# Optimization experiments

Measured on AMD Instinct MI355X. Metric: run time of the kernel, lower is better.

## Reference

```python
import jax, jax.numpy as jnp
import numpy as np
import math

B, T = 512, 512
ENC = 512          # 2 * input_size
N_MELS, R = 80, 2
ATTN, DEC = 256, 256
PRE_H, PRE_O = 256, 256
HID = 128          # DCA hidden
SC, SK = 8, 21     # static channels / kernel
DC, DK = 8, 21     # dynamic channels / kernel
PL, PA, PB = 11, 0.1, 0.9  # prior length, alpha, beta


def _betabinom_pmf(k, n, a, b):
    lg = math.lgamma
    return math.exp(lg(n + 1) - lg(k + 1) - lg(n - k + 1)
                    + lg(k + a) + lg(n - k + b) - lg(n + a + b)
                    - (lg(a) + lg(b) - lg(a + b)))


def setup_inputs() -> dict:
    key = jax.random.key(0)
    ks = iter(jax.random.split(key, 64))
    def rn(shape, s=0.05):
        return jax.random.normal(next(ks), shape, dtype=jnp.float32) * s
    inp = {}
    inp["h"] = rn([B, T, ENC], 1.0)
    inp["y"] = rn([B, N_MELS], 1.0)
    a = jax.random.uniform(next(ks), [B, T], dtype=jnp.float32)
    inp["alpha"] = a / a.sum(-1, keepdims=True)  # valid attention distribution
    inp["c"] = rn([B, ENC], 1.0)
    for n in ["attn_h0", "attn_c0", "rnn1_h0", "rnn1_c0", "rnn2_h0", "rnn2_c0"]:
        inp[n] = rn([B, ATTN], 1.0)
    # prenet
    inp["fc1_w"] = rn([PRE_H, N_MELS]); inp["fc1_b"] = rn([PRE_H])
    inp["fc2_w"] = rn([PRE_O, PRE_H]); inp["fc2_b"] = rn([PRE_O])
    # dynamic convolution attention
    inp["W_w"] = rn([HID, ATTN]); inp["W_b"] = rn([HID])
    inp["V_w"] = rn([DC * DK, HID])
    inp["F_w"] = rn([SC, 1, SK])
    inp["U_w"] = rn([HID, SC])
    inp["T_w"] = rn([HID, DC]); inp["T_b"] = rn([HID])
    inp["v_w"] = rn([1, HID])
    P = np.array([_betabinom_pmf(k, PL - 1, PA, PB) for k in range(PL)], np.float32)[::-1].copy()
    inp["P"] = jnp.asarray(P)
    # attn LSTM cell: input = 2*input_size + prenet output = 768
    inp["attn_wih"] = rn([4 * ATTN, ENC + PRE_O]); inp["attn_whh"] = rn([4 * ATTN, ATTN])
    inp["attn_bih"] = rn([4 * ATTN]); inp["attn_bhh"] = rn([4 * ATTN])
    inp["lin_w"] = rn([DEC, ENC + ATTN]); inp["lin_b"] = rn([DEC])
    for pfx in ["r1", "r2"]:
        inp[pfx + "_wih"] = rn([4 * DEC, DEC]); inp[pfx + "_whh"] = rn([4 * DEC, DEC])
        inp[pfx + "_bih"] = rn([4 * DEC]); inp[pfx + "_bhh"] = rn([4 * DEC])
    inp["proj_w"] = rn([N_MELS * R, DEC])
    return inp


def _lstm(x, h, c, wih, whh, bih, bhh):
    g = x @ wih.T + bih + h @ whh.T + bhh
    i, f, gg, o = jnp.split(g, 4, axis=-1)
    c2 = jax.nn.sigmoid(f) * c + jax.nn.sigmoid(i) * jnp.tanh(gg)
    return jax.nn.sigmoid(o) * jnp.tanh(c2), c2


def _win(x, k):
    # x: [B, T + k - 1] padded signal -> sliding windows [B, T, k]
    idx = jnp.arange(T)[:, None] + jnp.arange(k)[None, :]
    return x[:, idx]


def reference(h, y, alpha, c, attn_h0, attn_c0, rnn1_h0, rnn1_c0, rnn2_h0, rnn2_c0,
              fc1_w, fc1_b, fc2_w, fc2_b, W_w, W_b, V_w, F_w, U_w, T_w, T_b, v_w, P,
              attn_wih, attn_whh, attn_bih, attn_bhh, lin_w, lin_b,
              r1_wih, r1_whh, r1_bih, r1_bhh, r2_wih, r2_whh, r2_bih, r2_bhh, proj_w):
    # prenet (eval mode -> dropout inactive since fixed=False)
    yp = jax.nn.relu(jax.nn.relu(y @ fc1_w.T + fc1_b) @ fc2_w.T + fc2_b)
    attn_h, attn_c = _lstm(jnp.concatenate([c, yp], -1), attn_h0, attn_c0,
                           attn_wih, attn_whh, attn_bih, attn_bhh)
    # --- dynamic convolution attention ---
    # prior: causal conv with flipped beta-binomial pmf
    p = jnp.einsum('btk,k->bt', _win(jnp.pad(alpha, ((0, 0), (PL - 1, 0))), PL), P)
    p = jnp.log(jnp.clip(p, 1e-6))
    # dynamic filters per batch element: [B, DC, DK]
    G = (jnp.tanh(attn_h @ W_w.T + W_b) @ V_w.T).reshape(-1, DC, DK)
    wd = _win(jnp.pad(alpha, ((0, 0), ((DK - 1) // 2, (DK - 1) // 2))), DK)  # [B,T,DK]
    g = jnp.einsum('btk,bck->btc', wd, G)  # grouped conv1d, groups=B
    ws = _win(jnp.pad(alpha, ((0, 0), ((SK - 1) // 2, (SK - 1) // 2))), SK)
    f = jnp.einsum('btk,ck->btc', ws, F_w[:, 0, :])  # static conv1d
    e = jnp.squeeze(jnp.tanh(f @ U_w.T + g @ T_w.T + T_b) @ v_w.T, -1) + p
    alpha2 = jax.nn.softmax(e, axis=-1)
    # --- context + decoder stack ---
    c2 = jnp.einsum('bt,btd->bd', alpha2, h)
    x = jnp.concatenate([c2, attn_h], -1) @ lin_w.T + lin_b
    r1_h, r1_c = _lstm(x, rnn1_h0, rnn1_c0, r1_wih, r1_whh, r1_bih, r1_bhh)
    x = x + r1_h
    r2_h, r2_c = _lstm(x, rnn2_h0, rnn2_c0, r2_wih, r2_whh, r2_bih, r2_bhh)
    x = x + r2_h
    out = (x @ proj_w.T).reshape(-1, N_MELS, R)
    return (out, alpha2, c2, attn_h, attn_c, r1_h, r1_c, r2_h, r2_c)
```

## Files before the change

kernel.cpp:

```cpp
#include <hip/hip_runtime.h>

typedef unsigned short u16;
typedef __attribute__((ext_vector_type(8))) short s8v;
typedef __attribute__((ext_vector_type(4))) float f32x4;

__device__ __forceinline__ float bf2f(u16 u) { return __uint_as_float(((unsigned)u) << 16); }
__device__ __forceinline__ u16 f2bf(float f) {
    unsigned u = __float_as_uint(f);
    return (u16)((u + 0x7fffu + ((u >> 16) & 1u)) >> 16);
}
__device__ __forceinline__ float ldraw(const void* p, size_t i, int dt) {
    return dt ? ((const float*)p)[i] : bf2f(((const u16*)p)[i]);
}
__device__ __forceinline__ int fl(const int* F, int f) { return f < 0 ? 1 : F[f]; }
__device__ __forceinline__ float fast_tanh(float x) {
    x = fminf(fmaxf(x, -15.f), 15.f);
    float e = __expf(2.f * x);
    return (e - 1.f) / (e + 1.f);
}
__device__ __forceinline__ float sigm(float x) { return 1.f / (1.f + __expf(-x)); }

__global__ __launch_bounds__(256) void k_detect(int* __restrict__ flagsRaw,
    const void* p0, const void* p1, const void* p2, const void* p3, const void* p4,
    const void* p5, const void* p6, const void* p7, const void* p8, const void* p9,
    const void* p10, const void* p11, const void* p12, const void* p13, const void* p14,
    const void* p15, const void* p16, const void* p17, const void* p18, const void* p19,
    const void* p20, const void* p21, const void* p22, const void* p23, const void* p24,
    const void* p25, const void* p26, const void* p27, const void* p28, const void* p29,
    const void* p30, const void* p31, const void* p32, const void* p33, const void* p34,
    const void* p35, const void* p36, const void* p37)
{
    const void* ptrs[38] = {p0,p1,p2,p3,p4,p5,p6,p7,p8,p9,p10,p11,p12,p13,p14,p15,p16,
                            p17,p18,p19,p20,p21,p22,p23,p24,p25,p26,p27,p28,p29,p30,p31,
                            p32,p33,p34,p35,p36,p37};
    const int ns[38] = {134217728, 40960, 262144, 262144,
                        131072,131072,131072,131072,131072,131072,
                        20480,256,65536,256,
                        32768,128,21504,168,1024,1024,128,128,11,
                        786432,262144,1024,1024, 196608,256,
                        262144,262144,1024,1024, 262144,262144,1024,1024, 40960};
    __shared__ int s;
    int b = blockIdx.x, tid = threadIdx.x;
    if (tid == 0) s = 0;
    __syncthreads();
    int nsamp = ns[b] >> 1;
    if (nsamp > 512) nsamp = 512;
    const u16* q = (const u16*)ptrs[b];
    int bad = 0;
    for (int i = tid; i < nsamp; i += 256) {
        u16 u = q[2 * i];
        int e = (u >> 7) & 0xff;
        bad += (e < 96 || e > 159) ? 1 : 0;
    }
    atomicAdd(&s, bad);
    __syncthreads();
    if (tid == 0) flagsRaw[b] = (s * 4 > nsamp) ? 1 : 0;
}

__global__ __launch_bounds__(256) void k_finish(
    const int* __restrict__ FRAW, int* __restrict__ FF,
    const void* U_w, const void* T_w, const void* T_b, const void* v_w, const void* F_w,
    float* utw, float* tbf, float* vf, float* ff)
{
    __shared__ int sflag[38];
    const int big[38] = {1,1,1,1, 1,1,1,1,1,1, 1,0,1,0,
                         1,0,1,0,1,1,0,0,0, 1,1,1,1, 1,0,
                         1,1,1,1, 1,1,1,1, 1};
    int tid = threadIdx.x;
    if (tid == 0) {
        int s = 0, c = 0;
        for (int i = 0; i < 38; i++) if (big[i]) { s += FRAW[i]; c++; }
        int maj = (s * 2 > c) ? 1 : 0;
        for (int i = 0; i < 38; i++) { int v = big[i] ? FRAW[i] : maj; sflag[i] = v; FF[i] = v; }
    }
    __syncthreads();
    int dU = sflag[18], dT = sflag[19], dTb = sflag[20], dV = sflag[21], dF = sflag[17];
    for (int i = tid; i < 1024; i += 256) {
        int j = i >> 3, c = i & 7;
        utw[j * 16 + c]     = ldraw(U_w, i, dU);
        utw[j * 16 + 8 + c] = ldraw(T_w, i, dT);
    }
    if (tid < 128) { tbf[tid] = ldraw(T_b, tid, dTb); vf[tid] = ldraw(v_w, tid, dV); }
    if (tid < 168) ff[tid] = ldraw(F_w, tid, dF);
}

__device__ __forceinline__ void vg32_pair(const int* F,
    const void* A, int lda, int fa, const void* B, int ldb, int bo, int fb, int K,
    int m0, int n0, int N, int tid, int tx, int ty, float* acc,
    float (*As)[68], float (*Bs)[68])
{
    int dA = fl(F, fa), dB = fl(F, fb);
    bool fastp = dA && dB;
    for (int k0 = 0; k0 < K; k0 += 64) {
        __syncthreads();
        if (fastp) {
            #pragma unroll
            for (int p = 0; p < 2; p++) {
                int e = tid + p * 256;
                int row = e >> 4, kk = (e & 15) * 4;
                float4 va = {0.f, 0.f, 0.f, 0.f};
                if (k0 + kk < K)
                    va = *(const float4*)((const float*)A + (size_t)(m0 + row) * lda + k0 + kk);
                *(float4*)&As[row][kk] = va;
                int nr = n0 + row;
                float4 vb = {0.f, 0.f, 0.f, 0.f};
                if (nr < N && k0 + kk < K)
                    vb = *(const float4*)((const float*)B + (size_t)nr * ldb + bo + k0 + kk);
                *(float4*)&Bs[row][kk] = vb;
            }
        } else {
            #pragma unroll
            for (int p = 0; p < 8; p++) {
                int e = tid + p * 256;
                int row = e >> 6, kk = e & 63;
                As[row][kk] = (k0 + kk < K) ? ldraw(A, (size_t)(m0 + row) * lda + k0 + kk, dA) : 0.f;
                int nr = n0 + row;
                Bs[row][kk] = (nr < N && k0 + kk < K)
                            ? ldraw(B, (size_t)nr * ldb + bo + k0 + kk, dB) : 0.f;
            }
        }
        __syncthreads();
        #pragma unroll
        for (int kq = 0; kq < 16; kq++) {
            float4 a0 = *(const float4*)&As[ty][kq * 4];
            float4 a1 = *(const float4*)&As[ty + 16][kq * 4];
            float4 b0 = *(const float4*)&Bs[tx][kq * 4];
            float4 b1 = *(const float4*)&Bs[tx + 16][kq * 4];
            acc[0] += a0.x*b0.x + a0.y*b0.y + a0.z*b0.z + a0.w*b0.w;
            acc[1] += a0.x*b1.x + a0.y*b1.y + a0.z*b1.z + a0.w*b1.w;
            acc[2] += a1.x*b0.x + a1.y*b0.y + a1.z*b0.z + a1.w*b0.w;
            acc[3] += a1.x*b1.x + a1.y*b1.y + a1.z*b1.z + a1.w*b1.w;
        }
    }
}

__global__ __launch_bounds__(256) void k_vgemm32(
    const int* __restrict__ F,
    const void* A1, int lda1, int fa1, const void* B1, int ldb1, int bo1, int fb1, int K1,
    const void* A2, int lda2, int fa2, const void* B2, int ldb2, int bo2, int fb2, int K2,
    const void* bias1, int fx1,
    float* __restrict__ Cf, int ldc, int N, int act)
{
    __shared__ float As[32][68], Bs[32][68];
    int tid = threadIdx.x, tx = tid & 15, ty = tid >> 4;
    int m0 = blockIdx.y * 32, n0 = blockIdx.x * 32;
    float acc[4] = {0.f, 0.f, 0.f, 0.f};
    vg32_pair(F, A1, lda1, fa1, B1, ldb1, bo1, fb1, K1, m0, n0, N, tid, tx, ty, acc, As, Bs);
    if (A2) vg32_pair(F, A2, lda2, fa2, B2, ldb2, bo2, fb2, K2, m0, n0, N, tid, tx, ty, acc, As, Bs);

    #pragma unroll
    for (int c = 0; c < 2; c++) {
        int n = n0 + tx + c * 16;
        if (n >= N) continue;
        float bias = 0.f;
        if (bias1) bias += ldraw(bias1, n, fl(F, fx1));
        #pragma unroll
        for (int r = 0; r < 2; r++) {
            float v = acc[r * 2 + c] + bias;
            if (act == 1) v = fmaxf(v, 0.f);
            else if (act == 2) v = fast_tanh(v);
            Cf[(size_t)(m0 + ty + r * 16) * ldc + n] = v;
        }
    }
}

__global__ __launch_bounds__(256) void k_lin(
    const int* __restrict__ F, const float* __restrict__ part, float* __restrict__ o_c2,
    const float* __restrict__ ah, const void* lin_w, const void* lin_b,
    float* __restrict__ x1f)
{
    __shared__ float As[32][68], Bs[32][68];
    int tid = threadIdx.x, tx = tid & 15, ty = tid >> 4;
    int m0 = blockIdx.y * 32, n0 = blockIdx.x * 32;
    int dB = fl(F, 27);
    float acc[4] = {0.f, 0.f, 0.f, 0.f};
    for (int k0 = 0; k0 < 512; k0 += 64) {
        __syncthreads();
        #pragma unroll
        for (int p = 0; p < 2; p++) {
            int e = tid + p * 256;
            int row = e >> 4, kk = (e & 15) * 4;
            size_t idx = (size_t)(m0 + row) * 512 + k0 + kk;
            float4 va = *(const float4*)(part + idx);
            float4 vb2 = *(const float4*)(part + idx + 262144);
            va.x += vb2.x; va.y += vb2.y; va.z += vb2.z; va.w += vb2.w;
            *(float4*)&As[row][kk] = va;
            if (blockIdx.x == 0) *(float4*)(o_c2 + idx) = va;
            int nr = n0 + row;
            float4 vb;
            if (dB) {
                vb = *(const float4*)((const float*)lin_w + (size_t)nr * 768 + k0 + kk);
            } else {
                const u16* q = (const u16*)lin_w + (size_t)nr * 768 + k0 + kk;
                vb.x = bf2f(q[0]); vb.y = bf2f(q[1]); vb.z = bf2f(q[2]); vb.w = bf2f(q[3]);
            }
            *(float4*)&Bs[row][kk] = vb;
        }
        __syncthreads();
        #pragma unroll
        for (int kq = 0; kq < 16; kq++) {
            float4 a0 = *(const float4*)&As[ty][kq * 4];
            float4 a1 = *(const float4*)&As[ty + 16][kq * 4];
            float4 b0 = *(const float4*)&Bs[tx][kq * 4];
            float4 b1 = *(const float4*)&Bs[tx + 16][kq * 4];
            acc[0] += a0.x*b0.x + a0.y*b0.y + a0.z*b0.z + a0.w*b0.w;
            acc[1] += a0.x*b1.x + a0.y*b1.y + a0.z*b1.z + a0.w*b1.w;
            acc[2] += a1.x*b0.x + a1.y*b0.y + a1.z*b0.z + a1.w*b0.w;
            acc[3] += a1.x*b1.x + a1.y*b1.y + a1.z*b1.z + a1.w*b1.w;
        }
    }
    vg32_pair(F, ah, 256, -1, lin_w, 768, 512, 27, 256, m0, n0, 256, tid, tx, ty, acc, As, Bs);

    int dbias = fl(F, 28);
    #pragma unroll
    for (int c = 0; c < 2; c++) {
        int n = n0 + tx + c * 16;
        float bias = ldraw(lin_b, n, dbias);
        #pragma unroll
        for (int r = 0; r < 2; r++)
            x1f[(size_t)(m0 + ty + r * 16) * 256 + n] = acc[r * 2 + c] + bias;
    }
}

__device__ __forceinline__ void lstm_mfma_piece(const int* F,
    const void* A, int lda, int fa, const void* B, int ldb, int bo, int fb, int K,
    int b0, int j0, int tid, int wave, int lane, f32x4& acc,
    u16 (*As)[72], u16 (*Bs)[72])
{
    int dA = fl(F, fa), dB = fl(F, fb);
    for (int k0 = 0; k0 < K; k0 += 64) {
        __syncthreads();
        for (int g = tid; g < 640; g += 256) {
            const void* src; int dt; size_t idx; u16* dst;
            if (g < 128) {
                int row = g >> 3, kg = (g & 7) * 8;
                idx = (size_t)(b0 + row) * lda + k0 + kg;
                src = A; dt = dA; dst = &As[row][kg];
            } else {
                int gb = g - 128;
                int row = gb >> 3, kg = (gb & 7) * 8;
                int grow = (row >> 4) * 256 + j0 + (row & 15);
                idx = (size_t)grow * ldb + bo + k0 + kg;
                src = B; dt = dB; dst = &Bs[row][kg];
            }
            if (dt) {
                const float* sp = (const float*)src + idx;
                float4 a = *(const float4*)sp;
                float4 b = *(const float4*)(sp + 4);
                s8v v;
                v[0] = (short)f2bf(a.x); v[1] = (short)f2bf(a.y);
                v[2] = (short)f2bf(a.z); v[3] = (short)f2bf(a.w);
                v[4] = (short)f2bf(b.x); v[5] = (short)f2bf(b.y);
                v[6] = (short)f2bf(b.z); v[7] = (short)f2bf(b.w);
                *(s8v*)dst = v;
            } else {
                *(s8v*)dst = *(const s8v*)((const u16*)src + idx);
            }
        }
        __syncthreads();
        int r = lane & 15, kg = (lane >> 4) * 8;
        s8v a0 = *(const s8v*)&As[r][kg];
        s8v w0 = *(const s8v*)&Bs[wave * 16 + r][kg];
        acc = __builtin_amdgcn_mfma_f32_16x16x32_bf16(a0, w0, acc, 0, 0, 0);
        s8v a1 = *(const s8v*)&As[r][32 + kg];
        s8v w1 = *(const s8v*)&Bs[wave * 16 + r][32 + kg];
        acc = __builtin_amdgcn_mfma_f32_16x16x32_bf16(a1, w1, acc, 0, 0, 0);
    }
}

__global__ __launch_bounds__(256) void k_lstm(
    const int* __restrict__ F,
    const void* A1, int lda1, int fa1, const void* B1, int ldb1, int bo1, int fb1, int K1,
    const void* A2, int lda2, int fa2, const void* B2, int ldb2, int bo2, int fb2, int K2,
    const void* A3, int lda3, int fa3, const void* B3, int ldb3, int bo3, int fb3, int K3,
    const void* bih, int fx1, const void* bhh, int fx2,
    const void* c0, int fc0,
    float* __restrict__ h_out, float* __restrict__ c_out,
    const float* __restrict__ xprev, float* __restrict__ xout)
{
    __shared__ u16 As[16][72];
    __shared__ u16 Bs[64][72];
    __shared__ float sG[4][16][16];
    int tid = threadIdx.x, lane = tid & 63, wave = tid >> 6;
    int j0 = blockIdx.x * 16, b0 = blockIdx.y * 16;
    f32x4 acc = {0.f, 0.f, 0.f, 0.f};
    lstm_mfma_piece(F, A1, lda1, fa1, B1, ldb1, bo1, fb1, K1, b0, j0, tid, wave, lane, acc, As, Bs);
    if (A2) lstm_mfma_piece(F, A2, lda2, fa2, B2, ldb2, bo2, fb2, K2, b0, j0, tid, wave, lane, acc, As, Bs);
    if (A3) lstm_mfma_piece(F, A3, lda3, fa3, B3, ldb3, bo3, fb3, K3, b0, j0, tid, wave, lane, acc, As, Bs);

    #pragma unroll
    for (int r2 = 0; r2 < 4; r2++)
        sG[wave][(lane >> 4) * 4 + r2][lane & 15] = acc[r2];
    __syncthreads();

    int jl = tid & 15, bl = tid >> 4;
    int j = j0 + jl, b = b0 + bl;
    int dx1 = fl(F, fx1), dx2 = fl(F, fx2);
    float gi = sG[0][bl][jl] + ldraw(bih, j, dx1)       + ldraw(bhh, j, dx2);
    float gf = sG[1][bl][jl] + ldraw(bih, j + 256, dx1) + ldraw(bhh, j + 256, dx2);
    float gg = sG[2][bl][jl] + ldraw(bih, j + 512, dx1) + ldraw(bhh, j + 512, dx2);
    float go = sG[3][bl][jl] + ldraw(bih, j + 768, dx1) + ldraw(bhh, j + 768, dx2);
    size_t idx = (size_t)b * 256 + j;
    float cp = ldraw(c0, idx, F[fc0]);
    float cn = sigm(gf) * cp + sigm(gi) * fast_tanh(gg);
    float hn = sigm(go) * fast_tanh(cn);
    h_out[idx] = hn;
    c_out[idx] = cn;
    if (xprev) xout[idx] = xprev[idx] + hn;
}

__global__ __launch_bounds__(256) void k_dca(
    const int* __restrict__ F, const void* __restrict__ alpha, const void* __restrict__ P,
    const float* __restrict__ G, const float* __restrict__ utw, const float* __restrict__ tbf,
    const float* __restrict__ vf, const float* __restrict__ ff,
    float* __restrict__ o_a2)
{
    __shared__ float4 sut[512];
    __shared__ float stb[128], sv[128], sff[168], sgd[168], sal[532], spf[16], sred[8];
    int dA = F[2], dP = F[22];
    int b = blockIdx.x, tid = threadIdx.x;
    for (int i = tid; i < 512; i += 256) sut[i] = ((const float4*)utw)[i];
    if (tid < 128) { stb[tid] = tbf[tid]; sv[tid] = vf[tid]; }
    if (tid < 168) { sff[tid] = ff[tid]; sgd[tid] = G[(size_t)b * 168 + tid]; }
    if (tid < 11)  spf[tid] = ldraw(P, tid, dP);
    for (int i = tid; i < 532; i += 256)
        sal[i] = (i >= 10 && i < 522) ? ldraw(alpha, (size_t)b * 512 + i - 10, dA) : 0.f;
    __syncthreads();

    float e[2];
    #pragma unroll
    for (int q = 0; q < 2; q++) {
        int t = tid + q * 256;
        float aw[21];
        #pragma unroll
        for (int k = 0; k < 21; k++) aw[k] = sal[t + k];
        float pv = 0.f;
        #pragma unroll
        for (int k = 0; k < 11; k++) pv += aw[k] * spf[k];
        float fc[8], gc[8];
        #pragma unroll
        for (int c = 0; c < 8; c++) {
            float s1 = 0.f, s2 = 0.f;
            #pragma unroll
            for (int k = 0; k < 21; k++) {
                s1 += aw[k] * sff[c * 21 + k];
                s2 += aw[k] * sgd[c * 21 + k];
            }
            fc[c] = s1; gc[c] = s2;
        }
        float ev = 0.f;
        #pragma unroll 4
        for (int j = 0; j < 128; j++) {
            float4 u0 = sut[j * 4 + 0], u1 = sut[j * 4 + 1];
            float4 t0 = sut[j * 4 + 2], t1 = sut[j * 4 + 3];
            float a = stb[j];
            a += fc[0] * u0.x + fc[1] * u0.y + fc[2] * u0.z + fc[3] * u0.w;
            a += fc[4] * u1.x + fc[5] * u1.y + fc[6] * u1.z + fc[7] * u1.w;
            a += gc[0] * t0.x + gc[1] * t0.y + gc[2] * t0.z + gc[3] * t0.w;
            a += gc[4] * t1.x + gc[5] * t1.y + gc[6] * t1.z + gc[7] * t1.w;
            ev += fast_tanh(a) * sv[j];
        }
        e[q] = ev + __logf(fmaxf(pv, 1e-6f));
    }

    float m = fmaxf(e[0], e[1]);
    #pragma unroll
    for (int off = 32; off >= 1; off >>= 1) m = fmaxf(m, __shfl_xor(m, off));
    if ((tid & 63) == 0) sred[tid >> 6] = m;
    __syncthreads();
    m = fmaxf(fmaxf(sred[0], sred[1]), fmaxf(sred[2], sred[3]));
    float x0 = __expf(e[0] - m), x1 = __expf(e[1] - m);
    float s = x0 + x1;
    #pragma unroll
    for (int off = 32; off >= 1; off >>= 1) s += __shfl_xor(s, off);
    if ((tid & 63) == 0) sred[4 + (tid >> 6)] = s;
    __syncthreads();
    s = sred[4] + sred[5] + sred[6] + sred[7];
    float inv = 1.f / s;
    o_a2[(size_t)b * 512 + tid]       = x0 * inv;
    o_a2[(size_t)b * 512 + tid + 256] = x1 * inv;
}

__global__ __launch_bounds__(256) void k_c2_part(
    const int* __restrict__ F, const float* __restrict__ a2,
    const void* __restrict__ h, float* __restrict__ part)
{
    int dH = F[0];
    int bi = blockIdx.x;
    int b = bi >> 1, sp = bi & 1;
    int tid = threadIdx.x;
    int dsub = (tid & 63) * 8;
    int tsub = tid >> 6;
    __shared__ float sa[256];
    sa[tid] = a2[(size_t)b * 512 + sp * 256 + tid];
    __syncthreads();
    float acc[8];
    #pragma unroll
    for (int j = 0; j < 8; j++) acc[j] = 0.f;
    size_t rowbase = (size_t)b * 512 + sp * 256;
    if (dH) {
        const float* hf = (const float*)h;
        for (int tt = tsub; tt < 256; tt += 4) {
            float a = sa[tt];
            const float* p = hf + (rowbase + tt) * 512 + dsub;
            float4 v0 = *(const float4*)p, v1 = *(const float4*)(p + 4);
            acc[0] += a * v0.x; acc[1] += a * v0.y; acc[2] += a * v0.z; acc[3] += a * v0.w;
            acc[4] += a * v1.x; acc[5] += a * v1.y; acc[6] += a * v1.z; acc[7] += a * v1.w;
        }
    } else {
        const u16* hb = (const u16*)h;
        for (int tt = tsub; tt < 256; tt += 4) {
            float a = sa[tt];
            const u16* p = hb + (rowbase + tt) * 512 + dsub;
            #pragma unroll
            for (int j = 0; j < 8; j++) acc[j] += a * bf2f(p[j]);
        }
    }
    __shared__ float sacc[256 * 8];
    #pragma unroll
    for (int j = 0; j < 8; j++) sacc[tid * 8 + j] = acc[j];
    __syncthreads();
    if (tid < 64) {
        float* pp = part + ((size_t)sp * 512 + b) * 512 + tid * 8;
        #pragma unroll
        for (int j = 0; j < 8; j++)
            pp[j] = sacc[tid * 8 + j] + sacc[(tid + 64) * 8 + j]
                  + sacc[(tid + 128) * 8 + j] + sacc[(tid + 192) * 8 + j];
    }
}

__global__ void k_plant_direct(float* out0, float v) {
    if (threadIdx.x == 0 && blockIdx.x == 0) out0[0] = v;
}

extern "C" void kernel_launch(void* const* d_in, const int* in_sizes, int n_in,
                              void* d_out, int out_size, void* d_ws, size_t ws_size,
                              hipStream_t stream)
{
    (void)out_size; (void)ws_size;
    float* outf = (float*)d_out;

    static const int exp_sizes[38] = {
        134217728, 40960, 262144, 262144,
        131072,131072,131072,131072,131072,131072,
        20480,256,65536,256,
        32768,128,21504,168,1024,1024,128,128,11,
        786432,262144,1024,1024, 196608,256,
        262144,262144,1024,1024, 262144,262144,1024,1024, 40960};
    int bad = 0;
    if (n_in != 38) bad = 100;
    else for (int i = 0; i < 38; i++)
        if (in_sizes[i] != exp_sizes[i]) { bad = i + 1; break; }
    if (bad) {
        k_plant_direct<<<1, 1, 0, stream>>>(outf, 4194304.f + 65536.f * (float)bad);
        return;
    }

    const void* h_enc  = d_in[0];  const void* y      = d_in[1];
    const void* alpha  = d_in[2];  const void* c_in   = d_in[3];
    const void* ah0    = d_in[4];  const void* ac0    = d_in[5];
    const void* r1h0   = d_in[6];  const void* r1c0   = d_in[7];
    const void* r2h0   = d_in[8];  const void* r2c0   = d_in[9];
    const void* fc1_w  = d_in[10]; const void* fc1_b  = d_in[11];
    const void* fc2_w  = d_in[12]; const void* fc2_b  = d_in[13];
    const void* W_w    = d_in[14]; const void* W_b    = d_in[15];
    const void* V_w    = d_in[16]; const void* F_w    = d_in[17];
    const void* U_w    = d_in[18]; const void* T_w    = d_in[19];
    const void* T_b    = d_in[20]; const void* v_w    = d_in[21];
    const void* P      = d_in[22];
    const void* a_wih  = d_in[23]; const void* a_whh  = d_in[24];
    const void* a_bih  = d_in[25]; const void* a_bhh  = d_in[26];
    const void* lin_w  = d_in[27]; const void* lin_b  = d_in[28];
    const void* r1_wih = d_in[29]; const void* r1_whh = d_in[30];
    const void* r1_bih = d_in[31]; const void* r1_bhh = d_in[32];
    const void* r2_wih = d_in[33]; const void* r2_whh = d_in[34];
    const void* r2_bih = d_in[35]; const void* r2_bhh = d_in[36];
    const void* proj_w = d_in[37];

    char* ws = (char*)d_ws;
    int*   FRAW = (int*)  (ws + 0);
    int*   FF   = (int*)  (ws + 256);
    float* utw  = (float*)(ws + 1024);
    float* tbf  = (float*)(ws + 9216);
    float* vf   = (float*)(ws + 9728);
    float* ffs  = (float*)(ws + 10240);
    float* h1f  = (float*)(ws + 12288);
    float* ypf  = (float*)(ws + 536576);
    float* thf  = (float*)(ws + 1060864);
    float* Gdf  = (float*)(ws + 1323008);
    float* part = (float*)(ws + 1667072);

    float* o_out = outf + 0;
    float* o_a2  = outf + 81920;
    float* o_c2  = outf + 344064;
    float* o_ah  = outf + 606208;
    float* o_ac  = outf + 737280;
    float* o_r1h = outf + 868352;
    float* o_r1c = outf + 999424;
    float* o_r2h = outf + 1130496;
    float* o_r2c = outf + 1261568;

    const void* nv = nullptr;
    dim3 blk(256, 1, 1);

    k_detect<<<38, blk, 0, stream>>>(FRAW,
        d_in[0], d_in[1], d_in[2], d_in[3], d_in[4], d_in[5], d_in[6], d_in[7], d_in[8],
        d_in[9], d_in[10], d_in[11], d_in[12], d_in[13], d_in[14], d_in[15], d_in[16],
        d_in[17], d_in[18], d_in[19], d_in[20], d_in[21], d_in[22], d_in[23], d_in[24],
        d_in[25], d_in[26], d_in[27], d_in[28], d_in[29], d_in[30], d_in[31], d_in[32],
        d_in[33], d_in[34], d_in[35], d_in[36], d_in[37]);
    k_finish<<<1, blk, 0, stream>>>(FRAW, FF, U_w, T_w, T_b, v_w, F_w, utw, tbf, vf, ffs);

    k_vgemm32<<<dim3(8, 16), blk, 0, stream>>>(FF,
        y, 80, 1, fc1_w, 80, 0, 10, 80,
        nv, 0, -1, nv, 0, 0, -1, 0,
        fc1_b, 11, h1f, 256, 256, 1);
    k_vgemm32<<<dim3(8, 16), blk, 0, stream>>>(FF,
        h1f, 256, -1, fc2_w, 256, 0, 12, 256,
        nv, 0, -1, nv, 0, 0, -1, 0,
        fc2_b, 13, ypf, 256, 256, 1);

    k_lstm<<<dim3(16, 32), blk, 0, stream>>>(FF,
        c_in, 512, 3, a_wih, 768, 0, 23, 512,
        ypf, 256, -1, a_wih, 768, 512, 23, 256,
        ah0, 256, 4, a_whh, 256, 0, 24, 256,
        a_bih, 25, a_bhh, 26, ac0, 5, o_ah, o_ac, nullptr, nullptr);

    k_vgemm32<<<dim3(4, 16), blk, 0, stream>>>(FF,
        o_ah, 256, -1, W_w, 256, 0, 14, 256,
        nv, 0, -1, nv, 0, 0, -1, 0,
        W_b, 15, thf, 128, 128, 2);
    k_vgemm32<<<dim3(6, 16), blk, 0, stream>>>(FF,
        thf, 128, -1, V_w, 128, 0, 16, 128,
        nv, 0, -1, nv, 0, 0, -1, 0,
        nv, -1, Gdf, 168, 168, 0);

    k_dca<<<512, blk, 0, stream>>>(FF, alpha, P, Gdf, utw, tbf, vf, ffs, o_a2);

    k_c2_part<<<1024, blk, 0, stream>>>(FF, o_a2, h_enc, part);

    float* x1f = h1f;
    float* x2f = ypf;
    k_lin<<<dim3(8, 16), blk, 0, stream>>>(FF, part, o_c2, o_ah, lin_w, lin_b, x1f);

    k_lstm<<<dim3(16, 32), blk, 0, stream>>>(FF,
        x1f, 256, -1, r1_wih, 256, 0, 29, 256,
        r1h0, 256, 6, r1_whh, 256, 0, 30, 256,
        nv, 0, -1, nv, 0, 0, -1, 0,
        r1_bih, 31, r1_bhh, 32, r1c0, 7, o_r1h, o_r1c, x1f, x2f);

    float* x3f = h1f;
    k_lstm<<<dim3(16, 32), blk, 0, stream>>>(FF,
        x2f, 256, -1, r2_wih, 256, 0, 33, 256,
        r2h0, 256, 8, r2_whh, 256, 0, 34, 256,
        nv, 0, -1, nv, 0, 0, -1, 0,
        r2_bih, 35, r2_bhh, 36, r2c0, 9, o_r2h, o_r2c, x2f, x3f);

    k_vgemm32<<<dim3(5, 16), blk, 0, stream>>>(FF,
        x3f, 256, -1, proj_w, 256, 0, 37, 256,
        nv, 0, -1, nv, 0, 0, -1, 0,
        nv, -1, o_out, 160, 160, 0);
}
```

Before: 329.0 us.

## Restructure DCA energy loop to keep U/T weights in registers across timesteps

The DCA kernel now writes the per-timestep static and dynamic conv features to shared memory. It then reassigns work so each lane of a 32-lane group holds 4 hidden units' U/T weights in registers and loops over 64 timesteps. The partial energies are reduced with shuffles, replacing the previous scheme where every thread streamed all 128 hidden units' weights from shared memory for its own timesteps. The prior filter taps move into registers. The change adds a 32 KB shared buffer, a shuffle reduction per timestep and extra register pressure, which may lower occupancy.

Result: no change. 328.8 us (-0.1%).

```diff
diff --git a/kernel.cpp b/kernel.cpp
--- a/kernel.cpp
+++ b/kernel.cpp
@@ -315,19 +315,22 @@
     const float* __restrict__ vf, const float* __restrict__ ff,
     float* __restrict__ o_a2)
 {
-    __shared__ float4 sut[512];
-    __shared__ float stb[128], sv[128], sff[168], sgd[168], sal[532], spf[16], sred[8];
+    __shared__ float sFC[16][512];
+    __shared__ float sal[532];
+    __shared__ float spv[512];
+    __shared__ float se[512];
+    __shared__ float sff[168], sgd[168];
+    __shared__ float sred[8];
     int dA = F[2], dP = F[22];
     int b = blockIdx.x, tid = threadIdx.x;
-    for (int i = tid; i < 512; i += 256) sut[i] = ((const float4*)utw)[i];
-    if (tid < 128) { stb[tid] = tbf[tid]; sv[tid] = vf[tid]; }
     if (tid < 168) { sff[tid] = ff[tid]; sgd[tid] = G[(size_t)b * 168 + tid]; }
-    if (tid < 11)  spf[tid] = ldraw(P, tid, dP);
     for (int i = tid; i < 532; i += 256)
         sal[i] = (i >= 10 && i < 522) ? ldraw(alpha, (size_t)b * 512 + i - 10, dA) : 0.f;
-    __syncthreads();
-
-    float e[2];
+    float pfv[11];
+    #pragma unroll
+    for (int k = 0; k < 11; k++) pfv[k] = ldraw(P, k, dP);
+    __syncthreads();
+
     #pragma unroll
     for (int q = 0; q < 2; q++) {
         int t = tid + q * 256;
@@ -336,8 +339,8 @@
         for (int k = 0; k < 21; k++) aw[k] = sal[t + k];
         float pv = 0.f;
         #pragma unroll
-        for (int k = 0; k < 11; k++) pv += aw[k] * spf[k];
-        float fc[8], gc[8];
+        for (int k = 0; k < 11; k++) pv += aw[k] * pfv[k];
+        spv[t] = pv;
         #pragma unroll
         for (int c = 0; c < 8; c++) {
             float s1 = 0.f, s2 = 0.f;
@@ -346,30 +349,55 @@
                 s1 += aw[k] * sff[c * 21 + k];
                 s2 += aw[k] * sgd[c * 21 + k];
             }
-            fc[c] = s1; gc[c] = s2;
-        }
-        float ev = 0.f;
-        #pragma unroll 4
-        for (int j = 0; j < 128; j++) {
-            float4 u0 = sut[j * 4 + 0], u1 = sut[j * 4 + 1];
-            float4 t0 = sut[j * 4 + 2], t1 = sut[j * 4 + 3];
-            float a = stb[j];
-            a += fc[0] * u0.x + fc[1] * u0.y + fc[2] * u0.z + fc[3] * u0.w;
-            a += fc[4] * u1.x + fc[5] * u1.y + fc[6] * u1.z + fc[7] * u1.w;
-            a += gc[0] * t0.x + gc[1] * t0.y + gc[2] * t0.z + gc[3] * t0.w;
-            a += gc[4] * t1.x + gc[5] * t1.y + gc[6] * t1.z + gc[7] * t1.w;
-            ev += fast_tanh(a) * sv[j];
-        }
-        e[q] = ev + __logf(fmaxf(pv, 1e-6f));
-    }
-
-    float m = fmaxf(e[0], e[1]);
+            sFC[c][t] = s1;
+            sFC[8 + c][t] = s2;
+        }
+    }
+    __syncthreads();
+
+    int js = tid & 31, tg = tid >> 5;
+    float4 uu[16];
+    {
+        const float4* up = (const float4*)(utw + js * 64);
+        #pragma unroll
+        for (int r = 0; r < 16; r++) uu[r] = up[r];
+    }
+    float tb4[4], v4[4];
+    #pragma unroll
+    for (int r = 0; r < 4; r++) { tb4[r] = tbf[js * 4 + r]; v4[r] = vf[js * 4 + r]; }
+
+    for (int tt = 0; tt < 64; tt++) {
+        int t = tg * 64 + tt;
+        float fc2[8], gc2[8];
+        #pragma unroll
+        for (int c = 0; c < 8; c++) { fc2[c] = sFC[c][t]; gc2[c] = sFC[8 + c][t]; }
+        float ep = 0.f;
+        #pragma unroll
+        for (int r = 0; r < 4; r++) {
+            float4 u0 = uu[r * 4 + 0], u1 = uu[r * 4 + 1];
+            float4 t0 = uu[r * 4 + 2], t1 = uu[r * 4 + 3];
+            float a = tb4[r];
+            a += fc2[0]*u0.x + fc2[1]*u0.y + fc2[2]*u0.z + fc2[3]*u0.w;
+            a += fc2[4]*u1.x + fc2[5]*u1.y + fc2[6]*u1.z + fc2[7]*u1.w;
+            a += gc2[0]*t0.x + gc2[1]*t0.y + gc2[2]*t0.z + gc2[3]*t0.w;
+            a += gc2[4]*t1.x + gc2[5]*t1.y + gc2[6]*t1.z + gc2[7]*t1.w;
+            ep += fast_tanh(a) * v4[r];
+        }
+        #pragma unroll
+        for (int off = 16; off >= 1; off >>= 1) ep += __shfl_xor(ep, off);
+        if (js == 0) se[t] = ep;
+    }
+    __syncthreads();
+
+    float e0 = se[tid]       + __logf(fmaxf(spv[tid], 1e-6f));
+    float e1 = se[tid + 256] + __logf(fmaxf(spv[tid + 256], 1e-6f));
+    float m = fmaxf(e0, e1);
     #pragma unroll
     for (int off = 32; off >= 1; off >>= 1) m = fmaxf(m, __shfl_xor(m, off));
     if ((tid & 63) == 0) sred[tid >> 6] = m;
     __syncthreads();
     m = fmaxf(fmaxf(sred[0], sred[1]), fmaxf(sred[2], sred[3]));
-    float x0 = __expf(e[0] - m), x1 = __expf(e[1] - m);
+    float x0 = __expf(e0 - m), x1 = __expf(e1 - m);
     float s = x0 + x1;
     #pragma unroll
     for (int off = 32; off >= 1; off >>= 1) s += __shfl_xor(s, off);
```
